# Performance work log

Measured on AMD Instinct MI355X. Metric: run time of the kernel, lower is better.

The kernel has to match this reference:

```python
import jax, jax.numpy as jnp
import numpy as np

D = 256; H = 8; HD = D // H; NK = 32; NLAYERS = 4; FF = 4 * D
B = 8; M = 768; N = 128; LT = 64; T = M + N + LT
SCALE = 1.0 / float(np.sqrt(HD))


def layer_norm(x, s, b):
    mu = x.mean(-1, keepdims=True)
    var = ((x - mu) ** 2).mean(-1, keepdims=True)
    return (x - mu) * jax.lax.rsqrt(var + 1e-5) * s + b


def sine_embed(pos, d):
    # MTR gen_sineembed_for_position: half dims for y, half for x, interleaved sin/cos
    half = d // 2
    dim_t = jnp.power(10000.0, 2.0 * (jnp.arange(half) // 2).astype(jnp.float32) / half)
    scale = 2.0 * np.pi
    def inter(e):
        return jnp.stack([jnp.sin(e[:, 0::2]), jnp.cos(e[:, 1::2])], -1).reshape(e.shape[0], -1)
    ex = pos[:, 0:1] * scale / dim_t
    ey = pos[:, 1:2] * scale / dim_t
    return jnp.concatenate([inter(ey), inter(ex)], -1)


def setup_inputs() -> dict:
    key = jax.random.key(0)
    ks = jax.random.split(key, 24)
    s = 0.02
    inp = {
        'map_token': jax.random.normal(ks[0], (B, M, D), jnp.float32),
        'agent_token': jax.random.normal(ks[1], (B, N, D), jnp.float32),
        'light_token': jax.random.normal(ks[2], (B, LT, D), jnp.float32),
        'map_position': jax.random.uniform(ks[3], (B, M, 2), jnp.float32) * 100.0,
        'agent_position': jax.random.uniform(ks[4], (B, N, 2), jnp.float32) * 100.0,
        'light_position': jax.random.uniform(ks[5], (B, LT, 2), jnp.float32) * 100.0,
        'map_valid_mask': jnp.ones((B, M), bool),
        'agent_valid_mask': jnp.ones((B, N), bool),
        'light_valid_mask': jnp.ones((B, LT), bool),
        'Wq': jax.random.normal(ks[6], (NLAYERS, D, D), jnp.float32) * s,
        'bq': jnp.zeros((NLAYERS, D), jnp.float32),
        'Wk': jax.random.normal(ks[7], (NLAYERS, D, D), jnp.float32) * s,
        'bk': jnp.zeros((NLAYERS, D), jnp.float32),
        'Wv': jax.random.normal(ks[8], (NLAYERS, D, D), jnp.float32) * s,
        'bv': jnp.zeros((NLAYERS, D), jnp.float32),
        'Wo': jax.random.normal(ks[9], (NLAYERS, D, D), jnp.float32) * s,
        'bo': jnp.zeros((NLAYERS, D), jnp.float32),
        'W1': jax.random.normal(ks[10], (NLAYERS, D, FF), jnp.float32) * s,
        'b1': jnp.zeros((NLAYERS, FF), jnp.float32),
        'W2': jax.random.normal(ks[11], (NLAYERS, FF, D), jnp.float32) * s,
        'b2': jnp.zeros((NLAYERS, D), jnp.float32),
        'ln1_s': jnp.ones((NLAYERS, D), jnp.float32),
        'ln1_b': jnp.zeros((NLAYERS, D), jnp.float32),
        'ln2_s': jnp.ones((NLAYERS, D), jnp.float32),
        'ln2_b': jnp.zeros((NLAYERS, D), jnp.float32),
    }
    return inp


def reference(map_token, agent_token, light_token, map_position, agent_position, light_position,
              map_valid_mask, agent_valid_mask, light_valid_mask,
              Wq, bq, Wk, bk, Wv, bv, Wo, bo, W1, b1, W2, b2, ln1_s, ln1_b, ln2_s, ln2_b):
    x = jnp.concatenate([map_token, agent_token, light_token], 1)             # [B,T,D]
    pos = jnp.concatenate([map_position, agent_position, light_position], 1)[..., :2]  # [B,T,2]
    # all tokens valid -> masked compaction is a static reshape
    xs = x.reshape(B * T, D)
    ps = pos.reshape(B * T, 2)
    # KNN within each scene (includes self, like knn_batch_mlogk on same set)
    d2 = jnp.sum((pos[:, :, None, :] - pos[:, None, :, :]) ** 2, -1)          # [B,T,T]
    _, idx = jax.lax.top_k(-d2, NK)                                            # [B,T,NK] local indices
    idx = (idx + (jnp.arange(B) * T)[:, None, None]).reshape(B * T, NK)        # global flat indices
    pe = sine_embed(ps, D)                                                     # [B*T,D]
    out = xs
    for l in range(NLAYERS):
        qk = out + pe
        q = (qk @ Wq[l] + bq[l]).reshape(-1, H, HD)
        k = (qk @ Wk[l] + bk[l]).reshape(-1, H, HD)
        v = (out @ Wv[l] + bv[l]).reshape(-1, H, HD)
        kn = k[idx]                                                            # [BT,NK,H,HD] gather
        vn = v[idx]
        att = jax.nn.softmax(jnp.einsum('nhd,nkhd->nhk', q, kn) * SCALE, axis=-1)
        a = jnp.einsum('nhk,nkhd->nhd', att, vn).reshape(-1, D) @ Wo[l] + bo[l]
        out = layer_norm(out + a, ln1_s[l], ln1_b[l])
        ff = jax.nn.relu(out @ W1[l] + b1[l]) @ W2[l] + b2[l]
        out = layer_norm(out + ff, ln2_s[l], ln2_b[l])
    full = out.reshape(B, T, D)
    return full[:, :M], full[:, M:M + N], full[:, M + N:]
```

## Files before the change

kernel.cpp:

```cpp
#include <hip/hip_runtime.h>
#include <math.h>

#define BB 8
#define MTOK 768
#define NTOK 128
#define LTOK 64
#define TT 960
#define BT 7680
#define DD 256
#define HH 8
#define HD 32
#define KNN 32
#define FFD 1024
#define NLAYERS 4
#define SCALE_ATT 0.17677669529663687f

typedef __attribute__((ext_vector_type(8))) short bfrag_t;
typedef __attribute__((ext_vector_type(4))) float accfrag_t;

__device__ __forceinline__ float b2f(unsigned short u) {
  union { unsigned int i; float f; } c; c.i = ((unsigned int)u) << 16; return c.f;
}
__device__ __forceinline__ unsigned short f2b(float f) {
  union { float f; unsigned int i; } c; c.f = f;
  return (unsigned short)((c.i + 0x7fffu + ((c.i >> 16) & 1u)) >> 16);
}
__device__ __forceinline__ float load_elem(const void* p, size_t i, int f) {
  return f ? b2f(((const unsigned short*)p)[i]) : ((const float*)p)[i];
}
__device__ __forceinline__ size_t pk_addr(int row, int col, int nks) {
  return ((size_t)((row >> 4) * nks + (col >> 5)) << 9)
       + (size_t)(((((col >> 3) & 3) << 4) + (row & 15)) * 8 + (col & 7));
}
__device__ __forceinline__ int swiz_tok(int blk) { return (blk & 7) * TT + (blk >> 3); }

#define FB_BQ 0
#define FB_BK 1024
#define FB_BV 2048
#define FB_BO 3072
#define FB_B1 4096
#define FB_B2 8192
#define FB_LN1S 9216
#define FB_LN1B 10240
#define FB_LN2S 11264
#define FB_LN2B 12288
#define FB_TOTAL 13312
struct ParamSrc { const void* p[13]; };
__global__ __launch_bounds__(256)
void conv_misc_kernel(ParamSrc ps, const void* tok, int* flagout,
                      float* __restrict__ dst, float* __restrict__ posf) {
  __shared__ int cnt;
  if (threadIdx.x == 0) cnt = 0;
  __syncthreads();
  const unsigned short* u = (const unsigned short*)tok;
  int ok = 0;
  for (int i = threadIdx.x; i < 1024; i += 256) {
    int e = (u[i] >> 7) & 0xFF;
    if (e >= 100 && e <= 140) ok++;
  }
  atomicAdd(&cnt, ok);
  __syncthreads();
  int f = (cnt >= 922) ? 1 : 0;
  if (blockIdx.x == 0 && threadIdx.x == 0) *flagout = f;
  if (blockIdx.x < BB) {
    int b = blockIdx.x;
    for (int t = threadIdx.x; t < TT * 2; t += 256) {
      int tok2 = t >> 1, c = t & 1;
      const void* p; size_t idx;
      if (tok2 < MTOK)             { p = ps.p[10]; idx = (size_t)(b * MTOK + tok2) * 2 + c; }
      else if (tok2 < MTOK + NTOK) { p = ps.p[11]; idx = (size_t)(b * NTOK + tok2 - MTOK) * 2 + c; }
      else                         { p = ps.p[12]; idx = (size_t)(b * LTOK + tok2 - MTOK - NTOK) * 2 + c; }
      posf[((size_t)b * TT + tok2) * 2 + c] = load_elem(p, idx, f);
    }
    return;
  }
  int i = (blockIdx.x - BB) * 256 + threadIdx.x;
  if (i >= FB_TOTAL) return;
  int src; size_t off;
  if (i < 4096)      { src = i >> 10;              off = i & 1023; }
  else if (i < 8192) { src = 4;                    off = i - 4096; }
  else               { src = 5 + ((i - 8192) >> 10); off = (i - 8192) & 1023; }
  dst[i] = load_elem(ps.p[src], off, f);
}

__device__ __forceinline__ unsigned long long shfl_xor_u64(unsigned long long v, int m) {
  unsigned lo = (unsigned)v, hi = (unsigned)(v >> 32);
  lo = (unsigned)__shfl_xor((int)lo, m);
  hi = (unsigned)__shfl_xor((int)hi, m);
  return ((unsigned long long)hi << 32) | (unsigned long long)lo;
}
__device__ __forceinline__ unsigned long long shfl_u64(unsigned long long v, int srcLane) {
  unsigned lo = (unsigned)v, hi = (unsigned)(v >> 32);
  lo = (unsigned)__shfl((int)lo, srcLane);
  hi = (unsigned)__shfl((int)hi, srcLane);
  return ((unsigned long long)hi << 32) | (unsigned long long)lo;
}
__device__ __forceinline__ unsigned long long bitonic64(unsigned long long key, int lane) {
#pragma unroll
  for (int kk = 2; kk <= 64; kk <<= 1) {
#pragma unroll
    for (int j = kk >> 1; j > 0; j >>= 1) {
      unsigned long long other = shfl_xor_u64(key, j);
      bool small_ = (lane & j) == 0;
      bool dir = (lane & kk) == 0;
      bool keep = ((key < other) == (small_ == dir));
      key = keep ? key : other;
    }
  }
  return key;
}

struct PackSrc { const void* s[6]; };
__global__ __launch_bounds__(256)
void mega_kernel(PackSrc w, const void* mt, const void* at, const void* lt,
                 const float* __restrict__ posf, const int* __restrict__ flag,
                 unsigned short* __restrict__ Wqkvpk, unsigned short* __restrict__ Wopk,
                 unsigned short* __restrict__ W1pk, unsigned short* __restrict__ W2pk,
                 unsigned short* __restrict__ pe_b, float* __restrict__ out_f,
                 unsigned short* __restrict__ pk1, unsigned short* __restrict__ qkpk,
                 int* __restrict__ idx_out) {
  __shared__ float sx[TT], sy[TT];
  __shared__ unsigned long long cbuf[4][64];
  int bid = blockIdx.x;
  if (bid < 12288) {
    int f = *flag;
    int id = bid * 256 + threadIdx.x;
    if (id < 786432) {
      int layer = id / 196608, rest = id % 196608;
      int sel = rest >> 16, e = rest & 65535;
      int k = e >> 8, col = e & 255;
      const void* src = w.s[sel];
      size_t si = (size_t)layer * 65536 + e;
      Wqkvpk[(size_t)layer * 196608 + (size_t)sel * 65536 + pk_addr(col, k, 8)] =
          f ? ((const unsigned short*)src)[si] : f2b(((const float*)src)[si]);
    } else if (id < 1048576) {
      int off = id - 786432, layer = off >> 16, e = off & 65535;
      int k = e >> 8, col = e & 255;
      size_t si = (size_t)layer * 65536 + e;
      Wopk[(size_t)layer * 65536 + pk_addr(col, k, 8)] =
          f ? ((const unsigned short*)w.s[3])[si] : f2b(((const float*)w.s[3])[si]);
    } else if (id < 2097152) {
      int off = id - 1048576, layer = off >> 18, e = off & 262143;
      int k = e >> 10, col = e & 1023;
      size_t si = (size_t)layer * 262144 + e;
      W1pk[(size_t)layer * 262144 + pk_addr(col, k, 8)] =
          f ? ((const unsigned short*)w.s[4])[si] : f2b(((const float*)w.s[4])[si]);
    } else {
      int off = id - 2097152, layer = off >> 18, e = off & 262143;
      int k = e >> 8, col = e & 255;
      size_t si = (size_t)layer * 262144 + e;
      W2pk[(size_t)layer * 262144 + pk_addr(col, k, 32)] =
          f ? ((const unsigned short*)w.s[5])[si] : f2b(((const float*)w.s[5])[si]);
    }
    return;
  }
  if (bid < 19968) {
    int n = swiz_tok(bid - 12288), d = threadIdx.x;
    int b = n / TT, t = n - b * TT;
    int f = *flag;
    const void* src; size_t si;
    if (t < MTOK)              { src = mt; si = (size_t)(b * MTOK + t) * DD + d; }
    else if (t < MTOK + NTOK)  { src = at; si = (size_t)(b * NTOK + (t - MTOK)) * DD + d; }
    else                       { src = lt; si = (size_t)(b * LTOK + (t - MTOK - NTOK)) * DD + d; }
    float x = load_elem(src, si, f);
    float px = posf[((size_t)b * TT + t) * 2 + 0];
    float py = posf[((size_t)b * TT + t) * 2 + 1];
    float coord = (d < 128) ? py : px;
    int j = d & 127;
    float expo = (float)(2 * (j >> 1)) / 128.0f;
    float dim_t = powf(10000.0f, expo);
    float e = coord * 6.283185307179586f / dim_t;
    float p = (j & 1) ? cosf(e) : sinf(e);
    size_t o = (size_t)n * DD + d;
    pe_b[o] = f2b(p);
    out_f[o] = x;
    size_t pa = pk_addr(n, d, 8);
    pk1[pa] = f2b(x);
    qkpk[pa] = f2b(x + p);
    return;
  }
  int kb = bid - 19968;
  int b = kb & 7;
  int qbase = (kb >> 3) * 4;
  for (int t = threadIdx.x; t < TT; t += 256) {
    sx[t] = posf[((size_t)b * TT + t) * 2 + 0];
    sy[t] = posf[((size_t)b * TT + t) * 2 + 1];
  }
  __syncthreads();
  int wave = threadIdx.x >> 6, lane = threadIdx.x & 63;
  int t = qbase + wave;
  float qx = sx[t], qy = sy[t];

  unsigned long long k[15];
#pragma unroll
  for (int c = 0; c < 15; c++) {
    int j = c * 64 + lane;
    float dx = qx - sx[j], dy = qy - sy[j];
    float d2 = __fadd_rn(__fmul_rn(dx, dx), __fmul_rn(dy, dy));
    k[c] = ((unsigned long long)__float_as_uint(d2) << 32) | (unsigned)j;
  }
  unsigned long long lm = k[0];
#pragma unroll
  for (int c = 1; c < 15; c++) lm = (k[c] < lm) ? k[c] : lm;

  unsigned long long sm = bitonic64(lm, lane);
  unsigned long long thr = shfl_u64(sm, 31);

  int c_l = 0;
#pragma unroll
  for (int c = 0; c < 15; c++) c_l += (k[c] <= thr) ? 1 : 0;
  int inc = c_l;
#pragma unroll
  for (int o = 1; o < 64; o <<= 1) {
    int tt = __shfl_up(inc, o);
    inc += (lane >= o) ? tt : 0;
  }
  int total = __shfl(inc, 63);
  int pos = inc - c_l;

  if (total <= 64) {
    unsigned long long* wb = cbuf[wave];
#pragma unroll
    for (int c = 0; c < 15; c++) {
      if (k[c] <= thr) { wb[pos] = k[c]; pos++; }
    }
    unsigned long long cand = (lane < total) ? wb[lane] : ~0ull;
    cand = bitonic64(cand, lane);
    if (lane < KNN)
      idx_out[((size_t)(b * TT + t)) * KNN + lane] = b * TT + (int)(cand & 0xFFFFFFFFu);
  } else {
    unsigned res = 0;
    for (int i = 0; i < KNN; i++) {
      unsigned long long m = k[0];
#pragma unroll
      for (int c = 1; c < 15; c++) m = (k[c] < m) ? k[c] : m;
#pragma unroll
      for (int o = 32; o > 0; o >>= 1) {
        unsigned long long om = shfl_xor_u64(m, o);
        m = (om < m) ? om : m;
      }
      if (lane == i) res = (unsigned)(m & 0xFFFFFFFFu);
      int owner = (int)(m & 63u), ch = (int)(((unsigned)(m & 0xFFFFFFFFu)) >> 6);
      if (lane == owner) {
#pragma unroll
        for (int c = 0; c < 15; c++) if (c == ch) k[c] = ~0ull;
      }
    }
    if (lane < KNN)
      idx_out[((size_t)(b * TT + t)) * KNN + lane] = b * TT + (int)res;
  }
}

template<int NKS, int NT>
__device__ __forceinline__ void wavegemm(const unsigned short* __restrict__ Apk,
                                         const unsigned short* __restrict__ Bpk,
                                         int rb, int cb0, accfrag_t (&acc)[NT]) {
  const int lane = threadIdx.x & 63;
  accfrag_t z = {0.f, 0.f, 0.f, 0.f};
#pragma unroll
  for (int nt = 0; nt < NT; nt++) acc[nt] = z;
  const unsigned short* ap = Apk + ((size_t)rb * NKS * 512 + lane * 8);
  const unsigned short* bp = Bpk + ((size_t)cb0 * NKS * 512 + lane * 8);
#pragma unroll 4
  for (int ks = 0; ks < NKS; ks++) {
    bfrag_t a = *(const bfrag_t*)(ap + ks * 512);
#pragma unroll
    for (int nt = 0; nt < NT; nt++) {
      bfrag_t b = *(const bfrag_t*)(bp + (size_t)(nt * NKS + ks) * 512);
      acc[nt] = __builtin_amdgcn_mfma_f32_16x16x32_bf16(a, b, acc[nt], 0, 0, 0);
    }
  }
}

__global__ __launch_bounds__(256)
void qkv_kernel(const unsigned short* __restrict__ qkpk,
                const unsigned short* __restrict__ outpk,
                const unsigned short* __restrict__ Wl,
                const float* __restrict__ pb, int l,
                unsigned short* __restrict__ QKV) {
  int scene = blockIdx.x & 7, r = blockIdx.x >> 3;
  int rbg = r % 15, cgall = r / 15;
  int wave = threadIdx.x >> 6, lane = threadIdx.x & 63;
  int rb = scene * 60 + rbg * 4 + wave;
  int sel = cgall >> 2, cg = cgall & 3;
  const unsigned short* A = (sel < 2) ? qkpk : outpk;
  const unsigned short* B = Wl + sel * 65536;
  const float* bias = pb + sel * 1024 + l * 256;
  accfrag_t acc[4];
  wavegemm<8,4>(A, B, rb, cg * 4, acc);
  int l16 = lane & 15, lq = lane >> 4;
  unsigned short* C = QKV + (size_t)sel * BT * DD;
#pragma unroll
  for (int nt = 0; nt < 4; nt++) {
    int col = cg * 64 + nt * 16 + l16;
    float bv = bias[col];
#pragma unroll
    for (int r4 = 0; r4 < 4; r4++) {
      int row = rb * 16 + lq * 4 + r4;
      C[(size_t)row * DD + col] = f2b(acc[nt][r4] + bv);
    }
  }
}

template<bool LAST>
__global__ __launch_bounds__(256)
void layer_kernel(const unsigned short* __restrict__ QKVin,
                  const int* __restrict__ idx,
                  const unsigned short* __restrict__ Wo,
                  const unsigned short* __restrict__ W1,
                  const unsigned short* __restrict__ W2,
                  const unsigned short* __restrict__ Wn,
                  const float* __restrict__ bo,
                  const float* __restrict__ b1,
                  const float* __restrict__ b2,
                  const float* __restrict__ pb, int ln,
                  float* __restrict__ yf,
                  const unsigned short* __restrict__ pe_b,
                  const float* __restrict__ g1, const float* __restrict__ t1,
                  const float* __restrict__ g2, const float* __restrict__ t2,
                  unsigned short* __restrict__ QKVout,
                  void* __restrict__ dout, const int* __restrict__ flag) {
  __shared__ char uA[40960];
  __shared__ unsigned short apk[4096];
  __shared__ int nbAll[16][KNN];
  __shared__ float ps1[4][16], ps2[4][16];
  unsigned short (*kn)[DD + 8] = (unsigned short (*)[DD + 8])uA;
  unsigned short (*vn)[DD + 8] = (unsigned short (*)[DD + 8])(uA + 16896);
  float* qs = (float*)(uA + 33792);
  float (*att)[KNN] = (float (*)[KNN])(uA + 34816);
  unsigned short* xls = (unsigned short*)uA;
  unsigned short* hls = (unsigned short*)(uA + 8192);

  int scene = blockIdx.x & 7, rbs = blockIdx.x >> 3;
  int wave = threadIdx.x >> 6, lane = threadIdx.x & 63;
  int rb = scene * 60 + rbs;
  int n0 = rb * 16;
  int l16 = lane & 15, lq = lane >> 4;
  int tid = threadIdx.x;

  const unsigned short* Qp = QKVin;
  const unsigned short* Kp = QKVin + (size_t)BT * DD;
  const unsigned short* Vp = QKVin + 2 * (size_t)BT * DD;
  for (int i = tid; i < 16 * KNN; i += 256)
    nbAll[i >> 5][i & 31] = idx[(size_t)(n0 + (i >> 5)) * KNN + (i & 31)];
  __syncthreads();
  for (int t16 = 0; t16 < 16; t16++) {
    int n = n0 + t16;
    qs[tid] = b2f(Qp[(size_t)n * DD + tid]);
#pragma unroll
    for (int p = 0; p < 4; p++) {
      int e = p * 256 + tid;
      int r = e >> 5, c8 = (e & 31) * 8;
      int srow = nbAll[t16][r];
      *(uint4*)(&kn[r][c8]) = *(const uint4*)(Kp + (size_t)srow * DD + c8);
      *(uint4*)(&vn[r][c8]) = *(const uint4*)(Vp + (size_t)srow * DD + c8);
    }
    __syncthreads();
    int h = tid >> 5, kk = tid & 31;
    float dot = 0.0f;
#pragma unroll
    for (int d = 0; d < HD; d++) dot += qs[h * HD + d] * b2f(kn[kk][h * HD + d]);
    float sc = dot * SCALE_ATT;
    float mx = sc;
#pragma unroll
    for (int o = 16; o > 0; o >>= 1) mx = fmaxf(mx, __shfl_xor(mx, o, 32));
    float ex = expf(sc - mx);
    float sm = ex;
#pragma unroll
    for (int o = 16; o > 0; o >>= 1) sm += __shfl_xor(sm, o, 32);
    att[h][kk] = ex / sm;
    __syncthreads();
    int d = kk;
    float oacc = 0.0f;
#pragma unroll
    for (int k2 = 0; k2 < KNN; k2++) oacc += att[h][k2] * b2f(vn[k2][h * HD + d]);
    apk[pk_addr(t16, tid, 8)] = f2b(oacc);
    __syncthreads();
  }

  float resv[4][4];
#pragma unroll
  for (int nt = 0; nt < 4; nt++) {
    int col = wave * 64 + nt * 16 + l16;
#pragma unroll
    for (int r4 = 0; r4 < 4; r4++) {
      int row = rb * 16 + lq * 4 + r4;
      resv[nt][r4] = yf[(size_t)row * DD + col];
    }
  }

  accfrag_t acc[4];
  wavegemm<8,4>(apk, Wo, 0, wave * 4, acc);
  float y[4][4];
  float s[4] = {0.f, 0.f, 0.f, 0.f}, s2[4] = {0.f, 0.f, 0.f, 0.f};
#pragma unroll
  for (int nt = 0; nt < 4; nt++) {
    int col = wave * 64 + nt * 16 + l16;
    float bv = bo[col];
#pragma unroll
    for (int r4 = 0; r4 < 4; r4++) {
      float x = acc[nt][r4] + bv + resv[nt][r4];
      y[nt][r4] = x; s[r4] += x; s2[r4] += x * x;
    }
  }
#pragma unroll
  for (int o = 1; o < 16; o <<= 1) {
#pragma unroll
    for (int r4 = 0; r4 < 4; r4++) { s[r4] += __shfl_xor(s[r4], o); s2[r4] += __shfl_xor(s2[r4], o); }
  }
  if (l16 == 0) {
#pragma unroll
    for (int r4 = 0; r4 < 4; r4++) { ps1[wave][lq * 4 + r4] = s[r4]; ps2[wave][lq * 4 + r4] = s2[r4]; }
  }
  __syncthreads();
#pragma unroll
  for (int r4 = 0; r4 < 4; r4++) {
    int r16 = lq * 4 + r4;
    float ts  = ps1[0][r16] + ps1[1][r16] + ps1[2][r16] + ps1[3][r16];
    float ts2 = ps2[0][r16] + ps2[1][r16] + ps2[2][r16] + ps2[3][r16];
    float mu = ts * (1.0f / 256.0f);
    float var = ts2 * (1.0f / 256.0f) - mu * mu;
    float rstd = 1.0f / sqrtf(fmaxf(var, 0.f) + 1e-5f);
#pragma unroll
    for (int nt = 0; nt < 4; nt++) {
      int col = wave * 64 + nt * 16 + l16;
      float v = (y[nt][r4] - mu) * rstd * g1[col] + t1[col];
      y[nt][r4] = v;
      xls[pk_addr(r16, col, 8)] = f2b(v);
    }
  }
  __syncthreads();

#pragma unroll
  for (int i = 0; i < 4; i++) {
    int cg = wave * 4 + i;
    accfrag_t a2[4];
    wavegemm<8,4>(xls, W1, 0, cg * 4, a2);
#pragma unroll
    for (int nt = 0; nt < 4; nt++) {
      int col = cg * 64 + nt * 16 + l16;
      float bv = b1[col];
#pragma unroll
      for (int r4 = 0; r4 < 4; r4++)
        hls[pk_addr(lq * 4 + r4, col, 32)] = f2b(fmaxf(a2[nt][r4] + bv, 0.0f));
    }
  }
  __syncthreads();

  accfrag_t a3[4];
  wavegemm<32,4>(hls, W2, 0, wave * 4, a3);
  float v2[4][4];
  float s3[4] = {0.f, 0.f, 0.f, 0.f}, s4[4] = {0.f, 0.f, 0.f, 0.f};
#pragma unroll
  for (int nt = 0; nt < 4; nt++) {
    int col = wave * 64 + nt * 16 + l16;
    float bv = b2[col];
#pragma unroll
    for (int r4 = 0; r4 < 4; r4++) {
      float x = a3[nt][r4] + bv + y[nt][r4];
      v2[nt][r4] = x; s3[r4] += x; s4[r4] += x * x;
    }
  }
#pragma unroll
  for (int o = 1; o < 16; o <<= 1) {
#pragma unroll
    for (int r4 = 0; r4 < 4; r4++) { s3[r4] += __shfl_xor(s3[r4], o); s4[r4] += __shfl_xor(s4[r4], o); }
  }
  if (l16 == 0) {
#pragma unroll
    for (int r4 = 0; r4 < 4; r4++) { ps1[wave][lq * 4 + r4] = s3[r4]; ps2[wave][lq * 4 + r4] = s4[r4]; }
  }
  __syncthreads();
  unsigned short* qkls = hls;
  int fl = LAST ? *flag : 0;
#pragma unroll
  for (int r4 = 0; r4 < 4; r4++) {
    int r16 = lq * 4 + r4;
    float ts  = ps1[0][r16] + ps1[1][r16] + ps1[2][r16] + ps1[3][r16];
    float ts2 = ps2[0][r16] + ps2[1][r16] + ps2[2][r16] + ps2[3][r16];
    float mu = ts * (1.0f / 256.0f);
    float var = ts2 * (1.0f / 256.0f) - mu * mu;
    float rstd = 1.0f / sqrtf(fmaxf(var, 0.f) + 1e-5f);
#pragma unroll
    for (int nt = 0; nt < 4; nt++) {
      int col = wave * 64 + nt * 16 + l16;
      float yv = (v2[nt][r4] - mu) * rstd * g2[col] + t2[col];
      int row = rb * 16 + r16;
      if (!LAST) {
        yf[(size_t)row * DD + col] = yv;
        float q = yv + b2f(pe_b[(size_t)row * DD + col]);
        xls[pk_addr(r16, col, 8)] = f2b(yv);
        qkls[pk_addr(r16, col, 8)] = f2b(q);
      } else {
        int t = rbs * 16 + r16;
        size_t o;
        if (t < MTOK)             o = (size_t)(scene * MTOK + t) * DD + col;
        else if (t < MTOK + NTOK) o = (size_t)BB * MTOK * DD + (size_t)(scene * NTOK + (t - MTOK)) * DD + col;
        else                      o = (size_t)BB * MTOK * DD + (size_t)BB * NTOK * DD
                                    + (size_t)(scene * LTOK + (t - MTOK - NTOK)) * DD + col;
        if (fl) ((unsigned short*)dout)[o] = f2b(yv);
        else    ((float*)dout)[o] = yv;
      }
    }
  }

  if (!LAST) {
    __syncthreads();
#pragma unroll
    for (int i = 0; i < 3; i++) {
      int cgall = wave * 3 + i;
      int sel = cgall >> 2, cg = cgall & 3;
      const unsigned short* A = (sel < 2) ? qkls : xls;
      accfrag_t a4[4];
      wavegemm<8,4>(A, Wn + sel * 65536, 0, cg * 4, a4);
      const float* bias = pb + sel * 1024 + ln * 256;
      unsigned short* C = QKVout + (size_t)sel * BT * DD;
#pragma unroll
      for (int nt = 0; nt < 4; nt++) {
        int col = cg * 64 + nt * 16 + l16;
        float bv = bias[col];
#pragma unroll
        for (int r4 = 0; r4 < 4; r4++) {
          int row = rb * 16 + lq * 4 + r4;
          C[(size_t)row * DD + col] = f2b(a4[nt][r4] + bv);
        }
      }
    }
  }
}

extern "C" void kernel_launch(void* const* d_in, const int* in_sizes, int n_in,
                              void* d_out, int out_size, void* d_ws, size_t ws_size,
                              hipStream_t stream) {
  const void* map_tok   = d_in[0];
  const void* agent_tok = d_in[1];
  const void* light_tok = d_in[2];
  const void* map_pos   = d_in[3];
  const void* agent_pos = d_in[4];
  const void* light_pos = d_in[5];
  const void* Wq  = d_in[9];
  const void* bq  = d_in[10];
  const void* Wk  = d_in[11];
  const void* bk  = d_in[12];
  const void* Wv  = d_in[13];
  const void* bv  = d_in[14];
  const void* Wo  = d_in[15];
  const void* bo  = d_in[16];
  const void* W1  = d_in[17];
  const void* b1  = d_in[18];
  const void* W2  = d_in[19];
  const void* b2  = d_in[20];
  const void* ln1s = d_in[21];
  const void* ln1b = d_in[22];
  const void* ln2s = d_in[23];
  const void* ln2b = d_in[24];

  size_t off = 0;
  char* base = (char*)d_ws;
  auto take = [&](size_t bytes) { char* p = base + off; off += (bytes + 255) & ~(size_t)255; return (void*)p; };
  int*   flag  = (int*)take(256);
  float* posf  = (float*)take((size_t)BT * 2 * 4);
  float* pbuf  = (float*)take((size_t)FB_TOTAL * 4);
  unsigned short* pe_b = (unsigned short*)take((size_t)BT * DD * 2);
  float* out_f = (float*)take((size_t)BT * DD * 4);
  unsigned short* pk1  = (unsigned short*)take((size_t)BT * DD * 2);
  unsigned short* qkpk = (unsigned short*)take((size_t)BT * DD * 2);
  unsigned short* QKVa = (unsigned short*)take((size_t)3 * BT * DD * 2);
  unsigned short* QKVb = (unsigned short*)take((size_t)3 * BT * DD * 2);
  int* idxb = (int*)take((size_t)BT * KNN * 4);
  unsigned short* Wqkvpk = (unsigned short*)take((size_t)NLAYERS * 3 * DD * DD * 2);
  unsigned short* Wopk   = (unsigned short*)take((size_t)NLAYERS * DD * DD * 2);
  unsigned short* W1pk   = (unsigned short*)take((size_t)NLAYERS * DD * FFD * 2);
  unsigned short* W2pk   = (unsigned short*)take((size_t)NLAYERS * DD * FFD * 2);

  ParamSrc ps; ps.p[0]=bq; ps.p[1]=bk; ps.p[2]=bv; ps.p[3]=bo; ps.p[4]=b1;
  ps.p[5]=b2; ps.p[6]=ln1s; ps.p[7]=ln1b; ps.p[8]=ln2s; ps.p[9]=ln2b;
  ps.p[10]=map_pos; ps.p[11]=agent_pos; ps.p[12]=light_pos;
  conv_misc_kernel<<<BB + (FB_TOTAL + 255) / 256, 256, 0, stream>>>(ps, map_tok, flag, pbuf, posf);

  PackSrc pw; pw.s[0]=Wq; pw.s[1]=Wk; pw.s[2]=Wv; pw.s[3]=Wo; pw.s[4]=W1; pw.s[5]=W2;
  mega_kernel<<<21888, 256, 0, stream>>>(pw, map_tok, agent_tok, light_tok, posf, flag,
                                         Wqkvpk, Wopk, W1pk, W2pk,
                                         pe_b, out_f, pk1, qkpk, idxb);

  qkv_kernel<<<1440, 256, 0, stream>>>(qkpk, pk1, Wqkvpk, pbuf, 0, QKVa);

  for (int l = 0; l < NLAYERS; l++) {
    unsigned short* Qin  = (l & 1) ? QKVb : QKVa;
    unsigned short* Qout = (l & 1) ? QKVa : QKVb;
    if (l < NLAYERS - 1)
      layer_kernel<false><<<480, 256, 0, stream>>>(
          Qin, idxb,
          Wopk + (size_t)l * 65536, W1pk + (size_t)l * 262144, W2pk + (size_t)l * 262144,
          Wqkvpk + (size_t)(l + 1) * 196608,
          pbuf + FB_BO + l * 256, pbuf + FB_B1 + l * 1024, pbuf + FB_B2 + l * 256,
          pbuf, l + 1,
          out_f, pe_b,
          pbuf + FB_LN1S + l * 256, pbuf + FB_LN1B + l * 256,
          pbuf + FB_LN2S + l * 256, pbuf + FB_LN2B + l * 256,
          Qout, d_out, flag);
    else
      layer_kernel<true><<<480, 256, 0, stream>>>(
          Qin, idxb,
          Wopk + (size_t)l * 65536, W1pk + (size_t)l * 262144, W2pk + (size_t)l * 262144,
          Wqkvpk,
          pbuf + FB_BO + l * 256, pbuf + FB_B1 + l * 1024, pbuf + FB_B2 + l * 256,
          pbuf, 0,
          out_f, pe_b,
          pbuf + FB_LN1S + l * 256, pbuf + FB_LN1B + l * 256,
          pbuf + FB_LN2S + l * 256, pbuf + FB_LN2B + l * 256,
          Qout, d_out, flag);
  }
}
```

Baseline: 423.8 us.

## Compute neighbor attention per wave, reading K/V directly without block barriers

The attention stage is reorganized so that each wave handles its own query tokens, four per wave, instead of the whole block processing one token at a time. Previously every token staged its gathered K and V rows in LDS and paid three block-wide barriers. Now each lane computes a full Q·K dot product for one neighbor and head half straight from global memory, and the softmax probabilities pass through a small per-wave LDS scratch. The V accumulation reads 4-element slices directly from global memory, which removes most __syncthreads. The trade-off is more scattered uncoalesced global loads per lane and more register pressure.

Result: slower. 458.1 us (+8.1%).

```diff
diff --git a/kernel.cpp b/kernel.cpp
--- a/kernel.cpp
+++ b/kernel.cpp
@@ -324,10 +324,6 @@
   __shared__ unsigned short apk[4096];
   __shared__ int nbAll[16][KNN];
   __shared__ float ps1[4][16], ps2[4][16];
-  unsigned short (*kn)[DD + 8] = (unsigned short (*)[DD + 8])uA;
-  unsigned short (*vn)[DD + 8] = (unsigned short (*)[DD + 8])(uA + 16896);
-  float* qs = (float*)(uA + 33792);
-  float (*att)[KNN] = (float (*)[KNN])(uA + 34816);
   unsigned short* xls = (unsigned short*)uA;
   unsigned short* hls = (unsigned short*)(uA + 8192);
 
@@ -344,39 +340,58 @@
   for (int i = tid; i < 16 * KNN; i += 256)
     nbAll[i >> 5][i & 31] = idx[(size_t)(n0 + (i >> 5)) * KNN + (i & 31)];
   __syncthreads();
-  for (int t16 = 0; t16 < 16; t16++) {
-    int n = n0 + t16;
-    qs[tid] = b2f(Qp[(size_t)n * DD + tid]);
-#pragma unroll
-    for (int p = 0; p < 4; p++) {
-      int e = p * 256 + tid;
-      int r = e >> 5, c8 = (e & 31) * 8;
-      int srow = nbAll[t16][r];
-      *(uint4*)(&kn[r][c8]) = *(const uint4*)(Kp + (size_t)srow * DD + c8);
-      *(uint4*)(&vn[r][c8]) = *(const uint4*)(Vp + (size_t)srow * DD + c8);
-    }
-    __syncthreads();
-    int h = tid >> 5, kk = tid & 31;
-    float dot = 0.0f;
-#pragma unroll
-    for (int d = 0; d < HD; d++) dot += qs[h * HD + d] * b2f(kn[kk][h * HD + d]);
-    float sc = dot * SCALE_ATT;
-    float mx = sc;
-#pragma unroll
-    for (int o = 16; o > 0; o >>= 1) mx = fmaxf(mx, __shfl_xor(mx, o, 32));
-    float ex = expf(sc - mx);
-    float sm = ex;
-#pragma unroll
-    for (int o = 16; o > 0; o >>= 1) sm += __shfl_xor(sm, o, 32);
-    att[h][kk] = ex / sm;
-    __syncthreads();
-    int d = kk;
-    float oacc = 0.0f;
-#pragma unroll
-    for (int k2 = 0; k2 < KNN; k2++) oacc += att[h][k2] * b2f(vn[k2][h * HD + d]);
-    apk[pk_addr(t16, tid, 8)] = f2b(oacc);
-    __syncthreads();
-  }
+  {
+    float* attW = (float*)uA + wave * (8 * 33 + 4);
+    int j32 = lane & 31, half = lane >> 5;
+    int h2 = lane >> 3, d0 = (lane & 7) * 4;
+    for (int g = 0; g < 4; g++) {
+      int t16 = g * 4 + wave;
+      int n = n0 + t16;
+      int nbj = nbAll[t16][j32];
+      const bfrag_t* kr = (const bfrag_t*)(Kp + (size_t)nbj * DD + half * 128);
+      const bfrag_t* qr = (const bfrag_t*)(Qp + (size_t)n * DD + half * 128);
+      float att4[4];
+#pragma unroll
+      for (int h = 0; h < 4; h++) {
+        bfrag_t q0 = qr[h * 4 + 0], q1 = qr[h * 4 + 1], q2 = qr[h * 4 + 2], q3 = qr[h * 4 + 3];
+        bfrag_t k0 = kr[h * 4 + 0], k1 = kr[h * 4 + 1], k2 = kr[h * 4 + 2], k3 = kr[h * 4 + 3];
+        float dot = 0.0f;
+#pragma unroll
+        for (int e = 0; e < 8; e++) dot += b2f((unsigned short)q0[e]) * b2f((unsigned short)k0[e]);
+#pragma unroll
+        for (int e = 0; e < 8; e++) dot += b2f((unsigned short)q1[e]) * b2f((unsigned short)k1[e]);
+#pragma unroll
+        for (int e = 0; e < 8; e++) dot += b2f((unsigned short)q2[e]) * b2f((unsigned short)k2[e]);
+#pragma unroll
+        for (int e = 0; e < 8; e++) dot += b2f((unsigned short)q3[e]) * b2f((unsigned short)k3[e]);
+        float sc = dot * SCALE_ATT;
+        float mx = sc;
+#pragma unroll
+        for (int o = 16; o > 0; o >>= 1) mx = fmaxf(mx, __shfl_xor(mx, o, 32));
+        float ex = expf(sc - mx);
+        float sm = ex;
+#pragma unroll
+        for (int o = 16; o > 0; o >>= 1) sm += __shfl_xor(sm, o, 32);
+        att4[h] = ex / sm;
+      }
+#pragma unroll
+      for (int h = 0; h < 4; h++)
+        attW[(half * 4 + h) * 33 + j32] = att4[h];
+      float o4[4] = {0.f, 0.f, 0.f, 0.f};
+      for (int j = 0; j < KNN; j++) {
+        float a = attW[h2 * 33 + j];
+        int nv = nbAll[t16][j];
+        union { unsigned int u[2]; unsigned short s[4]; } vv;
+        *(uint2*)vv.u = *(const uint2*)(Vp + (size_t)nv * DD + h2 * HD + d0);
+#pragma unroll
+        for (int e = 0; e < 4; e++) o4[e] += a * b2f(vv.s[e]);
+      }
+      int col = h2 * HD + d0;
+      unsigned short* ap = apk + pk_addr(t16, col, 8);
+      ap[0] = f2b(o4[0]); ap[1] = f2b(o4[1]); ap[2] = f2b(o4[2]); ap[3] = f2b(o4[3]);
+    }
+  }
+  __syncthreads();
 
   float resv[4][4];
 #pragma unroll
```
